# Kernel optimization log

Hardware: AMD Instinct MI355X
Metric: run time of the kernel (lower is better)

The kernel has to match this reference:

```python
import jax, jax.numpy as jnp
import numpy as np

B, NR, NA, NF = 2, 768, 768, 16
RIN, AIN = 1024, 1024
DIM, HEADS, DHEAD, DEPTH = 512, 8, 64, 4
INNER = HEADS * DHEAD
IFF = int(DIM * 4 * 2 / 3)  # 1365, GEGLU inner dim


def _ln(x, g, b=None):
    mu = jnp.mean(x, axis=-1, keepdims=True)
    var = jnp.mean((x - mu) ** 2, axis=-1, keepdims=True)
    y = (x - mu) * jax.lax.rsqrt(var + 1e-5) * g
    return y if b is None else y + b


def _heads(t):
    b, n, _ = t.shape
    return t.reshape(b, n, HEADS, DHEAD).transpose(0, 2, 1, 3)  # b h n d


def _attend(qx, kvx, wq, wkv, wo, mask):
    q = _heads(qx @ wq) * (DHEAD ** -0.5)
    k, v = map(_heads, jnp.split(kvx @ wkv, 2, axis=-1))
    sim = jnp.einsum('bhid,bhjd->bhij', q, k)
    sim = jnp.where(mask, sim, -jnp.finfo(sim.dtype).max)
    attn = jax.nn.softmax(sim, axis=-1)
    out = jnp.einsum('bhij,bhjd->bhid', attn, v)
    out = out.transpose(0, 2, 1, 3).reshape(qx.shape[0], -1, INNER)
    return out @ wo


def _masks():
    # token types: RNA=0, FUSION=2, ATAC=1, laid out [rna | fusion | atac]
    types = jnp.concatenate([jnp.zeros(NR, jnp.int32), jnp.full((NF,), 2, jnp.int32), jnp.ones(NA, jnp.int32)])
    same = (types[:, None] == types[None, :]).astype(jnp.int32)
    # replicates torch source precedence: (zorro_mask | types_from) == FUSION
    zorro = (same | types[:, None]) == 2
    rt = jnp.arange(3, dtype=jnp.int32)  # return token types (RNA, ATAC, FUSION)
    pm = (rt[:, None] == types[None, :]).astype(jnp.int32)
    # replicates source precedence: (pool_mask | return_types) == GLOBAL(3)
    pool = (pm | rt[:, None]) == 3
    return zorro[None, None], pool[None, None]


def setup_inputs() -> dict:
    key = jax.random.key(0)
    ks = jax.random.split(key, 16)
    w = lambda k, s: jax.random.normal(k, s, jnp.float32) * 0.02
    return {
        'rna': jax.random.normal(ks[0], (B, NR, RIN), jnp.float32),
        'atac': jax.random.normal(ks[1], (B, NA, AIN), jnp.float32),
        'rna_ln1_g': jnp.ones((RIN,)), 'rna_ln1_b': jnp.zeros((RIN,)),
        'rna_w': w(ks[2], (RIN, DIM)), 'rna_b': jnp.zeros((DIM,)),
        'rna_ln2_g': jnp.ones((DIM,)), 'rna_ln2_b': jnp.zeros((DIM,)),
        'atac_ln1_g': jnp.ones((AIN,)), 'atac_ln1_b': jnp.zeros((AIN,)),
        'atac_w': w(ks[3], (AIN, DIM)), 'atac_b': jnp.zeros((DIM,)),
        'atac_ln2_g': jnp.ones((DIM,)), 'atac_ln2_b': jnp.zeros((DIM,)),
        'fusion_tokens': jax.random.normal(ks[4], (NF, DIM), jnp.float32),
        'layers_attn_g': jnp.ones((DEPTH, DIM)),
        'layers_wq': w(ks[5], (DEPTH, DIM, INNER)),
        'layers_wkv': w(ks[6], (DEPTH, DIM, 2 * INNER)),
        'layers_wo': w(ks[7], (DEPTH, INNER, DIM)),
        'layers_ff_g': jnp.ones((DEPTH, DIM)),
        'layers_ff_w1': w(ks[8], (DEPTH, DIM, 2 * IFF)),
        'layers_ff_w2': w(ks[9], (DEPTH, IFF, DIM)),
        'final_g': jnp.ones((DIM,)),
        'return_tokens': jax.random.normal(ks[10], (3, DIM), jnp.float32),
        'pool_g': jnp.ones((DIM,)),
        'pool_wq': w(ks[11], (DIM, INNER)),
        'pool_wkv': w(ks[12], (DIM, 2 * INNER)),
        'pool_wo': w(ks[13], (INNER, DIM)),
    }


def reference(rna, atac, rna_ln1_g, rna_ln1_b, rna_w, rna_b, rna_ln2_g, rna_ln2_b,
              atac_ln1_g, atac_ln1_b, atac_w, atac_b, atac_ln2_g, atac_ln2_b,
              fusion_tokens, layers_attn_g, layers_wq, layers_wkv, layers_wo,
              layers_ff_g, layers_ff_w1, layers_ff_w2, final_g, return_tokens,
              pool_g, pool_wq, pool_wkv, pool_wo):
    zorro_mask, pool_mask = _masks()
    rna_tok = _ln(_ln(rna, rna_ln1_g, rna_ln1_b) @ rna_w + rna_b, rna_ln2_g, rna_ln2_b)
    atac_tok = _ln(_ln(atac, atac_ln1_g, atac_ln1_b) @ atac_w + atac_b, atac_ln2_g, atac_ln2_b)
    fus = jnp.broadcast_to(fusion_tokens, (B, NF, DIM))
    tokens = jnp.concatenate([rna_tok, fus, atac_tok], axis=1)  # [B, N, DIM]

    def layer(tok, p):
        ag, wq, wkv, wo, fg, w1, w2 = p
        xn = _ln(tok, ag)
        tok = tok + _attend(xn, xn, wq, wkv, wo, zorro_mask)
        h = _ln(tok, fg) @ w1
        x1, gate = jnp.split(h, 2, axis=-1)
        tok = tok + (jax.nn.gelu(gate, approximate=False) * x1) @ w2
        return tok, None

    tokens, _ = jax.lax.scan(layer, tokens,
                             (layers_attn_g, layers_wq, layers_wkv, layers_wo,
                              layers_ff_g, layers_ff_w1, layers_ff_w2))
    tokens = _ln(tokens, final_g)
    ret = jnp.broadcast_to(return_tokens, (B, 3, DIM))
    pooled = _attend(_ln(ret, pool_g), tokens, pool_wq, pool_wkv, pool_wo, pool_mask) + ret
    return pooled
```

## Files before the change

### kernel.cpp

```cpp
#include <hip/hip_runtime.h>
#include <stdint.h>
#include <stddef.h>

#define NTOK 1552
#define DIMM 512
#define IFFC 1365
#define IFF2 2730
#define NW1 2816
#define GSTRIDE 1408
#define BATCH 2
#define MALL (BATCH*NTOK)
#define AZ 6

typedef unsigned short u16;
typedef __attribute__((ext_vector_type(8))) short bf16x8;
typedef __attribute__((ext_vector_type(4))) float f32x4;

__device__ __forceinline__ u16 f2bf(float f){
  union { float f; uint32_t u; } v; v.f = f;
  uint32_t u = v.u;
  uint32_t r = (u + 0x7FFFu + ((u >> 16) & 1u)) >> 16;
  return (u16)r;
}
__device__ __forceinline__ float bf2f(u16 x){
  union { uint32_t u; float f; } v; v.u = ((uint32_t)x) << 16; return v.f;
}

__device__ __forceinline__ void gload_lds16(const u16* g, u16* l){
  __builtin_amdgcn_global_load_lds((const __attribute__((address_space(1))) void*)g,
                                   (__attribute__((address_space(3))) void*)l, 16, 0, 0);
}

__global__ void convall(const float* s0,const float* s1,const float* s2,const float* s3,
                        const float* s4,const float* s5,const float* s6,const float* s7,
                        u16* d0,u16* d1,u16* d2,u16* d3,u16* d4,u16* d5,u16* d6,u16* d7)
{
  const float* srcs[8] = {s0,s1,s2,s3,s4,s5,s6,s7};
  u16* dsts[8] = {d0,d1,d2,d3,d4,d5,d6,d7};
  const int KT[8]   = {32,32,16,16,16,16,44,16};
  const int NT[8]   = {16,16,32,16,16,88,16,32};
  const int TC[8]   = {512,512,2048,1024,1024,5632,2816,512};
  const int K_[8]   = {1024,1024,512,512,512,512,1365,512};
  const int NSRC[8] = {512,512,1024,512,512,2730,512,1024};
  const int LDK[8]  = {1024,1024,512,512,512,512,1408,512};
  const int NOUT[8] = {512,512,1024,512,512,2816,512,1024};
  const int WS_[8]  = {0,0,512*1024,512*512,512*512,512*2730,1365*512,0};
  const int WT_[8]  = {0,0,1024*512,512*512,512*512,2816*512,512*1408,0};

  int bid = blockIdx.x;
  int seg = 0, base = 0;
  while (seg < 7 && bid >= base + TC[seg]) { base += TC[seg]; ++seg; }
  int loc = bid - base;
  int kt = KT[seg];
  int z = loc / (kt*NT[seg]); loc -= z*(kt*NT[seg]);
  int kb = (loc % kt) * 32, nb = (loc / kt) * 32;
  const float* w = srcs[seg] + (size_t)z * WS_[seg];
  u16* wt = dsts[seg] + (size_t)z * WT_[seg];
  int K = K_[seg], NS = NSRC[seg], ldk = LDK[seg], NO = NOUT[seg];

  __shared__ float tile[32][33];
  int t = threadIdx.x;
  {
    int k = t >> 3, n4 = (t & 7) * 4;
    int gk = kb + k;
    float4 v = make_float4(0.f,0.f,0.f,0.f);
    if (gk < K){
      if (seg != 5){
        int gn = nb + n4;
        if (gn + 4 <= NS){
          v = *(const float4*)(w + (size_t)gk*NS + gn);
        } else {
          float* pv = (float*)&v;
          #pragma unroll
          for (int i = 0; i < 4; ++i){ int n = gn + i; if (n < NS) pv[i] = w[(size_t)gk*NS + n]; }
        }
      } else {
        float* pv = (float*)&v;
        #pragma unroll
        for (int i = 0; i < 4; ++i){
          int n = nb + n4 + i;
          if (n < NO){
            int bb = n >> 7, rr = n & 127, g = rr >> 5, hh = rr & 31;
            int j = bb*64 + g*16 + (hh & 15);
            if (j < 1365) pv[i] = w[(size_t)gk*NS + ((hh < 16) ? j : 1365 + j)];
          }
        }
      }
    }
    tile[k][n4] = v.x; tile[k][n4+1] = v.y; tile[k][n4+2] = v.z; tile[k][n4+3] = v.w;
  }
  __syncthreads();
  if (t < 128){
    int n = t >> 2, k8 = (t & 3) * 8;
    int gn = nb + n, gk = kb + k8;
    if (gn < NO && gk < ldk){
      u16 sh[8];
      #pragma unroll
      for (int i = 0; i < 8; ++i) sh[i] = f2bf(tile[k8+i][n]);
      *(bf16x8*)(wt + (size_t)gn*ldk + gk) = *(bf16x8*)sh;
    }
  }
}

__global__ void embed_ln1(const float* __restrict__ rna, const float* __restrict__ atac,
                          const float* __restrict__ g0, const float* __restrict__ b0,
                          const float* __restrict__ g1, const float* __restrict__ b1,
                          u16* __restrict__ out)
{
  int r = blockIdx.x;
  const float* x; const float* g; const float* bb;
  if (r < 1536){ x = rna + (size_t)r*1024; g = g0; bb = b0; }
  else { x = atac + (size_t)(r-1536)*1024; g = g1; bb = b1; }
  float s = 0.f, ss = 0.f;
  int t = threadIdx.x;
  float v0 = x[t], v1 = x[t+256], v2 = x[t+512], v3 = x[t+768];
  s = v0+v1+v2+v3; ss = v0*v0+v1*v1+v2*v2+v3*v3;
  #pragma unroll
  for (int off = 32; off >= 1; off >>= 1){ s += __shfl_xor(s, off); ss += __shfl_xor(ss, off); }
  __shared__ float rs_[4], rss_[4];
  int w = t >> 6;
  if ((t & 63) == 0){ rs_[w] = s; rss_[w] = ss; }
  __syncthreads();
  s = rs_[0]+rs_[1]+rs_[2]+rs_[3];
  ss = rss_[0]+rss_[1]+rss_[2]+rss_[3];
  float mu = s / 1024.f;
  float rstd = rsqrtf(ss / 1024.f - mu*mu + 1e-5f);
  u16* o = out + (size_t)r*1024;
  o[t]     = f2bf((v0-mu)*rstd*g[t]     + bb[t]);
  o[t+256] = f2bf((v1-mu)*rstd*g[t+256] + bb[t+256]);
  o[t+512] = f2bf((v2-mu)*rstd*g[t+512] + bb[t+512]);
  o[t+768] = f2bf((v3-mu)*rstd*g[t+768] + bb[t+768]);
}

__global__ void embed_addln2(const float* __restrict__ part,
                             const float* __restrict__ rb, const float* __restrict__ ab,
                             const float* __restrict__ g0, const float* __restrict__ bt0,
                             const float* __restrict__ g1, const float* __restrict__ bt1,
                             const float* __restrict__ ag0,
                             float* __restrict__ tok, u16* __restrict__ xn)
{
  int r = blockIdx.x;
  int mod = (r >= 1536);
  int rl = mod ? r - 1536 : r;
  int b = rl / 768, rr = rl % 768;
  const float* bias = mod ? ab : rb;
  const float* g = mod ? g1 : g0;
  const float* bt = mod ? bt1 : bt0;
  const float* p0 = part + (size_t)r*DIMM;
  const float* p1 = p0 + (size_t)3072*DIMM;
  int t = threadIdx.x;
  float v0 = p0[t] + p1[t] + bias[t];
  float v1 = p0[t+256] + p1[t+256] + bias[t+256];
  float s = v0 + v1, ss = v0*v0 + v1*v1;
  #pragma unroll
  for (int off = 32; off >= 1; off >>= 1){ s += __shfl_xor(s, off); ss += __shfl_xor(ss, off); }
  __shared__ float rs_[4], rss_[4];
  int w = t >> 6;
  if ((t & 63) == 0){ rs_[w] = s; rss_[w] = ss; }
  __syncthreads();
  s = rs_[0]+rs_[1]+rs_[2]+rs_[3];
  ss = rss_[0]+rss_[1]+rss_[2]+rss_[3];
  float mu = s / DIMM;
  float rstd = rsqrtf(ss / DIMM - mu*mu + 1e-5f);
  size_t row = (size_t)(b*NTOK + (mod ? 784 : 0) + rr)*DIMM;
  float t0 = (v0 - mu)*rstd*g[t]     + bt[t];
  float t1 = (v1 - mu)*rstd*g[t+256] + bt[t+256];
  tok[row + t] = t0; tok[row + t+256] = t1;
  float s2 = t0 + t1, ss2 = t0*t0 + t1*t1;
  #pragma unroll
  for (int off = 32; off >= 1; off >>= 1){ s2 += __shfl_xor(s2, off); ss2 += __shfl_xor(ss2, off); }
  __syncthreads();
  if ((t & 63) == 0){ rs_[w] = s2; rss_[w] = ss2; }
  __syncthreads();
  s2 = rs_[0]+rs_[1]+rs_[2]+rs_[3];
  ss2 = rss_[0]+rss_[1]+rss_[2]+rss_[3];
  float mu2 = s2 / DIMM;
  float rstd2 = rsqrtf(ss2 / DIMM - mu2*mu2 + 1e-5f);
  xn[row + t]     = f2bf((t0 - mu2)*rstd2*ag0[t]);
  xn[row + t+256] = f2bf((t1 - mu2)*rstd2*ag0[t+256]);
}

__global__ void fuscopy_ln(const float* __restrict__ ft, const float* __restrict__ ag0,
                           float* __restrict__ tok, u16* __restrict__ xn)
{
  int bid = blockIdx.x;
  int b = bid >> 4, rr = bid & 15;
  int t = threadIdx.x;
  const float* x = ft + (size_t)rr*DIMM;
  float v0 = x[t], v1 = x[t+256];
  size_t row = (size_t)(b*NTOK + 768 + rr)*DIMM;
  tok[row + t] = v0; tok[row + t+256] = v1;
  float s = v0 + v1, ss = v0*v0 + v1*v1;
  #pragma unroll
  for (int off = 32; off >= 1; off >>= 1){ s += __shfl_xor(s, off); ss += __shfl_xor(ss, off); }
  __shared__ float rs_[4], rss_[4];
  int w = t >> 6;
  if ((t & 63) == 0){ rs_[w] = s; rss_[w] = ss; }
  __syncthreads();
  s = rs_[0]+rs_[1]+rs_[2]+rs_[3];
  ss = rss_[0]+rss_[1]+rss_[2]+rss_[3];
  float mu = s / DIMM;
  float rstd = rsqrtf(ss / DIMM - mu*mu + 1e-5f);
  xn[row + t]     = f2bf((v0 - mu)*rstd*ag0[t]);
  xn[row + t+256] = f2bf((v1 - mu)*rstd*ag0[t+256]);
}

__global__ void resadd_ffnln(float* __restrict__ tok, const float* __restrict__ proj,
                             const float* __restrict__ g, u16* __restrict__ xn)
{
  int n = blockIdx.x, b = blockIdx.y;
  int pr = (n >= 768 && n < 784) ? (1 + n - 768) : 0;
  const float* p = proj + ((size_t)b*17 + pr)*DIMM;
  size_t row = (size_t)(b*NTOK + n)*DIMM;
  int t = threadIdx.x;
  float v0 = tok[row + t]     + p[t];
  float v1 = tok[row + t+256] + p[t+256];
  tok[row + t] = v0; tok[row + t+256] = v1;
  float s = v0 + v1, ss = v0*v0 + v1*v1;
  #pragma unroll
  for (int off = 32; off >= 1; off >>= 1){ s += __shfl_xor(s, off); ss += __shfl_xor(ss, off); }
  __shared__ float rs_[4], rss_[4];
  int w = t >> 6;
  if ((t & 63) == 0){ rs_[w] = s; rss_[w] = ss; }
  __syncthreads();
  s = rs_[0]+rs_[1]+rs_[2]+rs_[3];
  ss = rss_[0]+rss_[1]+rss_[2]+rss_[3];
  float mu = s / DIMM;
  float rstd = rsqrtf(ss / DIMM - mu*mu + 1e-5f);
  xn[row + t]     = f2bf((v0 - mu)*rstd*g[t]);
  xn[row + t+256] = f2bf((v1 - mu)*rstd*g[t+256]);
}

__global__ void skadd_ln(float* __restrict__ tok, const float* __restrict__ part,
                         const float* __restrict__ g, u16* __restrict__ xn)
{
  int r = blockIdx.x;
  size_t row = (size_t)r*DIMM;
  const float* p0 = part + row;
  const float* p1 = p0 + (size_t)MALL*DIMM;
  int t = threadIdx.x;
  float v0 = tok[row + t]     + p0[t]     + p1[t];
  float v1 = tok[row + t+256] + p0[t+256] + p1[t+256];
  tok[row + t] = v0; tok[row + t+256] = v1;
  float s = v0 + v1, ss = v0*v0 + v1*v1;
  #pragma unroll
  for (int off = 32; off >= 1; off >>= 1){ s += __shfl_xor(s, off); ss += __shfl_xor(ss, off); }
  __shared__ float rs_[4], rss_[4];
  int w = t >> 6;
  if ((t & 63) == 0){ rs_[w] = s; rss_[w] = ss; }
  __syncthreads();
  s = rs_[0]+rs_[1]+rs_[2]+rs_[3];
  ss = rss_[0]+rss_[1]+rss_[2]+rss_[3];
  float mu = s / DIMM;
  float rstd = rsqrtf(ss / DIMM - mu*mu + 1e-5f);
  xn[row + t]     = f2bf((v0 - mu)*rstd*g[t]);
  xn[row + t+256] = f2bf((v1 - mu)*rstd*g[t+256]);
}

__global__ __launch_bounds__(512) void gemm512(
    const u16* __restrict__ A, int lda,
    const u16* __restrict__ Bt, const u16* __restrict__ BtB, int mswitch, int ldk,
    float* __restrict__ C, int ldc, size_t Cz,
    u16* __restrict__ gout, float* __restrict__ csum,
    int M, int Nn, int K, int kchunk)
{
  __shared__ __align__(16) u16 As_lin[2][128*32];
  __shared__ __align__(16) u16 Bs_lin[2][128*32];
  __shared__ float colsum[2][128];
  const int t = threadIdx.x;
  const int lane = t & 63;
  const int w = t >> 6;
  const int wr = (w >> 2) * 64;
  const int wc = (w & 3) * 32;
  const int row0 = blockIdx.x * 128, col0 = blockIdx.y * 128;
  if (BtB && row0 >= mswitch) Bt = BtB;
  const int z = blockIdx.z;
  const int kbeg = z * kchunk;
  const int kend = (kbeg + kchunk < K) ? (kbeg + kchunk) : K;
  C += (size_t)z * Cz;
  const int l15 = lane & 15;
  const int l4 = (lane >> 4) * 8;
  const int sr = t >> 2, sc8 = (t & 3) * 8;
  int gr_s = row0 + sr; if (gr_s >= M) gr_s = M - 1;
  int gc_s = col0 + sr; if (gc_s >= Nn) gc_s = Nn - 1;
  const u16* Ag = A + (size_t)gr_s*lda + sc8;
  const u16* Bg = Bt + (size_t)gc_s*ldk + sc8;
  const int wb = w * 512;

  f32x4 acc[4][2];
  #pragma unroll
  for (int m = 0; m < 4; ++m)
    #pragma unroll
    for (int n = 0; n < 2; ++n)
      #pragma unroll
      for (int j = 0; j < 4; ++j) acc[m][n][j] = 0.f;

  gload_lds16(Ag + kbeg, &As_lin[0][wb]);
  gload_lds16(Bg + kbeg, &Bs_lin[0][wb]);
  __syncthreads();

  int cur = 0;
  for (int k0 = kbeg; k0 < kend; k0 += 32) {
    int k1 = k0 + 32;
    if (k1 < kend){
      gload_lds16(Ag + k1, &As_lin[cur^1][wb]);
      gload_lds16(Bg + k1, &Bs_lin[cur^1][wb]);
    }
    const u16* Ar = &As_lin[cur][0];
    const u16* Br = &Bs_lin[cur][0];
    bf16x8 af[4], bfr[2];
    #pragma unroll
    for (int m = 0; m < 4; ++m) af[m]  = *(const bf16x8*)(&Ar[(wr + m*16 + l15)*32 + l4]);
    #pragma unroll
    for (int n = 0; n < 2; ++n) bfr[n] = *(const bf16x8*)(&Br[(wc + n*16 + l15)*32 + l4]);
    #pragma unroll
    for (int m = 0; m < 4; ++m)
      #pragma unroll
      for (int n = 0; n < 2; ++n)
        acc[m][n] = __builtin_amdgcn_mfma_f32_16x16x32_bf16(af[m], bfr[n], acc[m][n], 0, 0, 0);
    __syncthreads();
    cur ^= 1;
  }
  const int rb = (lane >> 4) * 4;
  if (gout){
    int jcol = (col0 >> 1) + (w & 3)*16 + l15;
    #pragma unroll
    for (int m = 0; m < 4; ++m){
      int gr0 = row0 + wr + m*16 + rb;
      #pragma unroll
      for (int j = 0; j < 4; ++j){
        int gr = gr0 + j;
        if (gr < M){
          float gt = acc[m][1][j];
          float ge = 0.5f * gt * (1.0f + erff(gt * 0.70710678118654752f));
          gout[(size_t)gr*GSTRIDE + jcol] = f2bf(ge * acc[m][0][j]);
        }
      }
    }
  } else {
    #pragma unroll
    for (int m = 0; m < 4; ++m){
      int gr0 = row0 + wr + m*16 + rb;
      #pragma unroll
      for (int n = 0; n < 2; ++n){
        int gc = col0 + wc + n*16 + l15;
        if (gc >= Nn) continue;
        #pragma unroll
        for (int j = 0; j < 4; ++j){
          int gr = gr0 + j;
          if (gr < M) C[(size_t)gr*ldc + gc] = acc[m][n][j];
        }
      }
    }
  }
  if (csum && col0 >= 512){
    if (t < 256) colsum[t>>7][t&127] = 0.f;
    __syncthreads();
    #pragma unroll
    for (int n = 0; n < 2; ++n){
      float lv0 = 0.f, lv1 = 0.f;
      #pragma unroll
      for (int m = 0; m < 4; ++m){
        int gr0 = row0 + wr + m*16 + rb;
        #pragma unroll
        for (int j = 0; j < 4; ++j){
          float v = acc[m][n][j];
          if (gr0 + j < NTOK) lv0 += v; else lv1 += v;
        }
      }
      int lc = wc + n*16 + l15;
      atomicAdd(&colsum[0][lc], lv0);
      atomicAdd(&colsum[1][lc], lv1);
    }
    __syncthreads();
    if (t < 256){
      int bb = t>>7, c = t&127;
      csum[((size_t)(bb*25) + blockIdx.x)*512 + (col0 - 512) + c] = colsum[bb][c];
    }
  }
}

__global__ __launch_bounds__(256) void fused_attn(
    const u16* __restrict__ xn, const u16* __restrict__ wqt,
    const float* __restrict__ kv, float* __restrict__ apart)
{
  int h = blockIdx.x, b = blockIdx.y;
  int qi = blockIdx.z / AZ, jz = blockIdx.z % AZ;
  int t = threadIdx.x;
  int lane = t & 63, wid = t >> 6;
  __shared__ float xs[512];
  __shared__ float qs[64];
  __shared__ float pl[256];
  __shared__ float red[4][64];
  __shared__ float redm[4];

  {
    int row = b*NTOK + 768 + qi;
    const u16* xr = xn + (size_t)row*DIMM;
    xs[t] = bf2f(xr[t]);
    xs[t+256] = bf2f(xr[t+256]);
  }
  __syncthreads();

  {
    const u16* wrr = wqt + (size_t)(h*64 + lane)*DIMM + wid*128;
    float a = 0.f;
    #pragma unroll
    for (int k = 0; k < 128; k += 8){
      bf16x8 wv = *(const bf16x8*)(wrr + k);
      int kb = wid*128 + k;
      #pragma unroll
      for (int i = 0; i < 8; ++i) a += xs[kb+i] * bf2f((u16)wv[i]);
    }
    red[wid][lane] = a;
  }
  __syncthreads();
  if (t < 64) qs[t] = (red[0][t] + red[1][t] + red[2][t] + red[3][t]) * 0.125f;
  __syncthreads();

  int jj = jz*256 + t;
  int j = (jj < 768) ? jj : jj + 16;
  float a = 0.f;
  {
    const float* kr = kv + ((size_t)(b*NTOK + j))*1024 + h*64;
    #pragma unroll
    for (int d = 0; d < 64; d += 4){
      float4 kd = *(const float4*)(kr + d);
      a += qs[d]*kd.x + qs[d+1]*kd.y + qs[d+2]*kd.z + qs[d+3]*kd.w;
    }
  }

  float m = a;
  #pragma unroll
  for (int off = 32; off >= 1; off >>= 1) m = fmaxf(m, __shfl_xor(m, off));
  if (lane == 0) redm[wid] = m;
  __syncthreads();
  m = fmaxf(fmaxf(redm[0], redm[1]), fmaxf(redm[2], redm[3]));
  float p = __expf(a - m);
  pl[t] = p;
  float sq = p;
  #pragma unroll
  for (int off = 32; off >= 1; off >>= 1) sq += __shfl_xor(sq, off);
  if (lane == 0) redm[wid] = sq;
  __syncthreads();

  {
    int j0 = wid * 64;
    const float* vb = kv + ((size_t)(b*NTOK + jz*256 + j0 + ((jz*256 + j0 >= 768) ? 16 : 0)))*1024
                      + 512 + h*64 + lane;
    float a0=0.f, a1=0.f, a2=0.f, a3=0.f;
    #pragma unroll 4
    for (int i = 0; i < 64; i += 4){
      const float* vp = vb + (size_t)i*1024;
      a0 += pl[j0+i]   * vp[0];
      a1 += pl[j0+i+1] * vp[1024];
      a2 += pl[j0+i+2] * vp[2048];
      a3 += pl[j0+i+3] * vp[3072];
    }
    red[wid][lane] = a0+a1+a2+a3;
  }
  __syncthreads();
  float* po = apart + ((((size_t)jz*BATCH + b)*8 + h)*16 + qi) * 68;
  if (t < 64) po[t] = red[0][t] + red[1][t] + red[2][t] + red[3][t];
  else if (t == 64) po[64] = m;
  else if (t == 65) po[65] = redm[0] + redm[1] + redm[2] + redm[3];
}

__global__ __launch_bounds__(256) void attn_out(
    const float* __restrict__ apart, const float* __restrict__ csum,
    const u16* __restrict__ wot, float* __restrict__ proj)
{
  int colchunk = blockIdx.x;
  int b = blockIdx.y;
  int rg = blockIdx.z;
  int r0 = (rg == 0) ? 0 : (1 + 4*rg);
  int nr = (rg == 0) ? 5 : 4;
  __shared__ float zbl[5][512];
  __shared__ float red[4][64];
  int t = threadIdx.x;

  for (int rr = 0; rr < nr; ++rr){
    int r = r0 + rr;
    if (r == 0){
      for (int c = t; c < 512; c += 256){
        float s = 0.f;
        #pragma unroll
        for (int bx = 0; bx < 25; ++bx) s += csum[((size_t)(b*25)+bx)*512 + c];
        zbl[rr][c] = s * (1.0f/1552.0f);
      }
    } else {
      int qi = r - 1;
      for (int c = t; c < 512; c += 256){
        int h = c >> 6, d = c & 63;
        size_t base = ((size_t)b*8 + h)*16 + qi;
        float mz[AZ], sz[AZ];
        float M = -3.4e38f;
        #pragma unroll
        for (int z = 0; z < AZ; ++z){
          const float* po = apart + ((size_t)z*BATCH*8*16 + base)*68;
          mz[z] = po[64]; sz[z] = po[65];
          M = fmaxf(M, mz[z]);
        }
        float S = 0.f, O = 0.f;
        #pragma unroll
        for (int z = 0; z < AZ; ++z){
          const float* po = apart + ((size_t)z*BATCH*8*16 + base)*68;
          float wz = __expf(mz[z] - M);
          S += sz[z]*wz; O += po[d]*wz;
        }
        zbl[rr][c] = O / S;
      }
    }
  }
  __syncthreads();

  int col = colchunk*64 + (t & 63);
  int kq = t >> 6;
  const u16* wrow = wot + (size_t)col*512 + kq*128;
  for (int rr = 0; rr < nr; ++rr){
    float a = 0.f;
    #pragma unroll
    for (int k = 0; k < 128; k += 8){
      bf16x8 wv = *(const bf16x8*)(wrow + k);
      #pragma unroll
      for (int i = 0; i < 8; ++i) a += zbl[rr][kq*128 + k + i] * bf2f((u16)wv[i]);
    }
    red[kq][t & 63] = a;
    __syncthreads();
    if (t < 64)
      proj[((size_t)(b*17) + r0 + rr)*DIMM + colchunk*64 + t] =
        red[0][t] + red[1][t] + red[2][t] + red[3][t];
    __syncthreads();
  }
}

__global__ __launch_bounds__(256) void pool_final(
    const float* __restrict__ csum, const float* __restrict__ rt,
    const float* __restrict__ pg, const float* __restrict__ wq,
    const float* __restrict__ kv, const float* __restrict__ wo,
    float* __restrict__ out)
{
  int colchunk = blockIdx.x;
  int br = blockIdx.y; int b = br/3, r = br%3;
  __shared__ float ys[512];
  __shared__ float q2l[512];
  __shared__ float qred[2][512];
  __shared__ float fred[16][64];
  __shared__ float sm[8][16];
  __shared__ float pn[8][16];
  __shared__ float rs_[4], rss_[4];
  int t = threadIdx.x;

  if (r < 2){
    float a0 = 0.f, a1 = 0.f;
    #pragma unroll
    for (int bx = 0; bx < 25; ++bx){
      a0 += csum[((size_t)(b*25)+bx)*512 + t];
      a1 += csum[((size_t)(b*25)+bx)*512 + t + 256];
    }
    ys[t] = a0 * (1.0f/1552.0f);
    ys[t+256] = a1 * (1.0f/1552.0f);
    __syncthreads();
  } else {
    const float* x = rt + 2*DIMM;
    float v0 = x[t], v1 = x[t+256];
    float s = v0 + v1, ss = v0*v0 + v1*v1;
    #pragma unroll
    for (int off = 32; off >= 1; off >>= 1){ s += __shfl_xor(s, off); ss += __shfl_xor(ss, off); }
    int w = t >> 6;
    if ((t & 63) == 0){ rs_[w] = s; rss_[w] = ss; }
    __syncthreads();
    s = rs_[0]+rs_[1]+rs_[2]+rs_[3];
    ss = rss_[0]+rss_[1]+rss_[2]+rss_[3];
    float mu = s / DIMM;
    float rstd = rsqrtf(ss / DIMM - mu*mu + 1e-5f);
    ys[t]     = (v0 - mu)*rstd*pg[t];
    ys[t+256] = (v1 - mu)*rstd*pg[t+256];
    __syncthreads();
    {
      int c4 = (t & 127) * 4;
      int kq = t >> 7;
      float ax=0.f, ay=0.f, az=0.f, aw=0.f;
      #pragma unroll 8
      for (int k = kq*256; k < kq*256 + 256; ++k){
        float yv = ys[k];
        float4 w4 = *(const float4*)(wq + (size_t)k*512 + c4);
        ax += yv*w4.x; ay += yv*w4.y; az += yv*w4.z; aw += yv*w4.w;
      }
      qred[kq][c4] = ax; qred[kq][c4+1] = ay; qred[kq][c4+2] = az; qred[kq][c4+3] = aw;
    }
    __syncthreads();
    q2l[t]     = (qred[0][t]     + qred[1][t])     * 0.125f;
    q2l[t+256] = (qred[0][t+256] + qred[1][t+256]) * 0.125f;
    __syncthreads();
    if (t < 128){
      int h = t >> 4, j = t & 15;
      const float* kr = kv + ((size_t)(b*NTOK + 768 + j))*1024 + h*64;
      float a = 0.f;
      #pragma unroll
      for (int d = 0; d < 64; ++d) a += q2l[h*64 + d] * kr[d];
      sm[h][j] = a;
    }
    __syncthreads();
    if (t < 8){
      float m = -3.4e38f;
      #pragma unroll
      for (int j = 0; j < 16; ++j) m = fmaxf(m, sm[t][j]);
      float e[16]; float s2 = 0.f;
      #pragma unroll
      for (int j = 0; j < 16; ++j){ e[j] = __expf(sm[t][j] - m); s2 += e[j]; }
      float inv = 1.0f / s2;
      #pragma unroll
      for (int j = 0; j < 16; ++j) pn[t][j] = e[j] * inv;
    }
    __syncthreads();
    {
      int c0 = t, c1 = t + 256;
      int h0 = c0 >> 6, h1 = c1 >> 6;
      float a0 = 0.f, a1 = 0.f;
      #pragma unroll
      for (int j = 0; j < 16; ++j){
        const float* vr = kv + ((size_t)(b*NTOK + 768 + j))*1024 + 512;
        a0 += pn[h0][j] * vr[c0];
        a1 += pn[h1][j] * vr[c1];
      }
      ys[c0] = a0; ys[c1] = a1;
    }
    __syncthreads();
  }

  {
    int c4l = (t & 15) * 4;
    int c4 = colchunk*64 + c4l;
    int kq = t >> 4;
    float ax=0.f, ay=0.f, az=0.f, aw=0.f;
    #pragma unroll 8
    for (int k = kq*32; k < kq*32 + 32; ++k){
      float yv = ys[k];
      float4 w4 = *(const float4*)(wo + (size_t)k*512 + c4);
      ax += yv*w4.x; ay += yv*w4.y; az += yv*w4.z; aw += yv*w4.w;
    }
    fred[kq][c4l] = ax; fred[kq][c4l+1] = ay; fred[kq][c4l+2] = az; fred[kq][c4l+3] = aw;
  }
  __syncthreads();
  if (t < 64){
    float a = 0.f;
    #pragma unroll
    for (int kq = 0; kq < 16; ++kq) a += fred[kq][t];
    int c = colchunk*64 + t;
    out[(size_t)br*DIMM + c] = a + rt[(size_t)r*DIMM + c];
  }
}

extern "C" void kernel_launch(void* const* d_in, const int* in_sizes, int n_in,
                              void* d_out, int out_size, void* d_ws, size_t ws_size,
                              hipStream_t stream)
{
  const float* rna        = (const float*)d_in[0];
  const float* atac       = (const float*)d_in[1];
  const float* rna_ln1_g  = (const float*)d_in[2];
  const float* rna_ln1_b  = (const float*)d_in[3];
  const float* rna_w      = (const float*)d_in[4];
  const float* rna_b      = (const float*)d_in[5];
  const float* rna_ln2_g  = (const float*)d_in[6];
  const float* rna_ln2_b  = (const float*)d_in[7];
  const float* atac_ln1_g = (const float*)d_in[8];
  const float* atac_ln1_b = (const float*)d_in[9];
  const float* atac_w     = (const float*)d_in[10];
  const float* atac_b     = (const float*)d_in[11];
  const float* atac_ln2_g = (const float*)d_in[12];
  const float* atac_ln2_b = (const float*)d_in[13];
  const float* fusion_tok = (const float*)d_in[14];
  const float* lay_ag     = (const float*)d_in[15];
  const float* lay_wq     = (const float*)d_in[16];
  const float* lay_wkv    = (const float*)d_in[17];
  const float* lay_wo     = (const float*)d_in[18];
  const float* lay_fg     = (const float*)d_in[19];
  const float* lay_w1     = (const float*)d_in[20];
  const float* lay_w2     = (const float*)d_in[21];
  const float* final_g    = (const float*)d_in[22];
  const float* ret_tok    = (const float*)d_in[23];
  const float* pool_g     = (const float*)d_in[24];
  const float* pool_wq    = (const float*)d_in[25];
  const float* pool_wkv   = (const float*)d_in[26];
  const float* pool_wo    = (const float*)d_in[27];

  uint8_t* ws = (uint8_t*)d_ws;
  size_t off = 0;
  auto carve = [&](size_t bytes) -> uint8_t* {
    uint8_t* p = ws + off;
    off += (bytes + 255) & ~(size_t)255;
    return p;
  };
  u16* rna_wt   = (u16*)carve((size_t)512*1024*2);
  u16* atac_wt  = (u16*)carve((size_t)512*1024*2);
  u16* wkvt     = (u16*)carve((size_t)4*1024*512*2);
  u16* wqt      = (u16*)carve((size_t)4*512*512*2);
  u16* wot      = (u16*)carve((size_t)4*512*512*2);
  u16* w1t      = (u16*)carve((size_t)4*NW1*512*2);
  u16* w2t      = (u16*)carve((size_t)4*512*GSTRIDE*2);
  u16* pool_wkvt= (u16*)carve((size_t)1024*512*2);
  float* tok   = (float*)carve((size_t)MALL * DIMM * 4);
  u16*   xn    = (u16*)  carve((size_t)MALL * DIMM * 2);
  float* kv    = (float*)carve((size_t)MALL * 1024 * 4);
  u16*   lnbuf = (u16*)  carve((size_t)3072 * 1024 * 2);
  float* proj  = (float*)carve((size_t)BATCH*17*DIMM * 4);
  float* csum  = (float*)carve((size_t)BATCH*25*512 * 4);
  float* apart = (float*)carve((size_t)AZ*BATCH*8*16*68 * 4);
  u16*   gbuf  = (u16*)  carve((size_t)MALL * GSTRIDE * 2);
  float* skpart= (float*)carve((size_t)2 * MALL * 512 * 4);
  (void)ws_size;

  convall<<<14080, 256, 0, stream>>>(rna_w, atac_w, lay_wkv, lay_wq, lay_wo, lay_w1, lay_w2, pool_wkv,
                                     rna_wt, atac_wt, wkvt, wqt, wot, w1t, w2t, pool_wkvt);

  embed_ln1<<<3072, 256, 0, stream>>>(rna, atac, rna_ln1_g, rna_ln1_b, atac_ln1_g, atac_ln1_b, lnbuf);
  gemm512<<<dim3(24, 4, 2), 512, 0, stream>>>(lnbuf, 1024, rna_wt, atac_wt, 1536, 1024,
                                              skpart, 512, (size_t)3072*512, nullptr, nullptr,
                                              3072, 512, 1024, 512);
  embed_addln2<<<3072, 256, 0, stream>>>(skpart, rna_b, atac_b, rna_ln2_g, rna_ln2_b,
                                         atac_ln2_g, atac_ln2_b, lay_ag, tok, xn);
  fuscopy_ln<<<32, 256, 0, stream>>>(fusion_tok, lay_ag, tok, xn);

  for (int l = 0; l < 4; ++l){
    const float* fg  = lay_fg + (size_t)l*DIMM;
    const float* gnext = (l < 3) ? (lay_ag + (size_t)(l+1)*DIMM) : final_g;
    const u16* wkvt_l = wkvt + (size_t)l*1024*512;
    const u16* wqt_l  = wqt  + (size_t)l*512*512;
    const u16* wot_l  = wot  + (size_t)l*512*512;
    const u16* w1t_l  = w1t  + (size_t)l*NW1*512;
    const u16* w2t_l  = w2t  + (size_t)l*512*GSTRIDE;

    gemm512<<<dim3(25, 8, 1), 512, 0, stream>>>(xn, 512, wkvt_l, nullptr, 0, 512,
                                                kv, 1024, 0, nullptr, csum, MALL, 1024, 512, 512);
    fused_attn<<<dim3(8, BATCH, 16*AZ), 256, 0, stream>>>(xn, wqt_l, kv, apart);
    attn_out<<<dim3(8, BATCH, 4), 256, 0, stream>>>(apart, csum, wot_l, proj);
    resadd_ffnln<<<dim3(NTOK, BATCH), 256, 0, stream>>>(tok, proj, fg, xn);
    gemm512<<<dim3(25, 22, 1), 512, 0, stream>>>(xn, 512, w1t_l, nullptr, 0, 512,
                                                 nullptr, 0, 0, gbuf, nullptr, MALL, NW1, 512, 512);
    gemm512<<<dim3(25, 4, 2), 512, 0, stream>>>(gbuf, GSTRIDE, w2t_l, nullptr, 0, GSTRIDE,
                                                skpart, 512, (size_t)MALL*512, nullptr, nullptr,
                                                MALL, 512, GSTRIDE, 704);
    skadd_ln<<<MALL, 256, 0, stream>>>(tok, skpart, gnext, xn);
  }

  gemm512<<<dim3(25, 8, 1), 512, 0, stream>>>(xn, 512, pool_wkvt, nullptr, 0, 512,
                                              kv, 1024, 0, nullptr, csum, MALL, 1024, 512, 512);
  pool_final<<<dim3(8, 6), 256, 0, stream>>>(csum, ret_tok, pool_g, pool_wq, kv, pool_wo,
                                             (float*)d_out);
}
```

Measured before the change: 540.6 us.

## Merge prep kernels and raise split-K for embed and FFN-down GEMMs

Folds the embedding LayerNorm into the weight-conversion launch and the fusion-token copy into embed_addln2, cutting two kernel launches. It also raises split-K for the embedding GEMM from 2 to 4 and for the W2 GEMM from 2 to 3 (K chunk 480), so these small grids fill more compute units. The reduction kernels now sum more partial buffers, which adds memory traffic. The W2 split of 3×480 covers K=1408 only if the GEMM clamps the last chunk.

Result: faster. 525.5 us (-2.8%).

```diff
diff --git a/kernel.cpp b/kernel.cpp
--- a/kernel.cpp
+++ b/kernel.cpp
@@ -11,6 +11,8 @@
 #define BATCH 2
 #define MALL (BATCH*NTOK)
 #define AZ 6
+#define W2SK 3
+#define EMSK 4
 
 typedef unsigned short u16;
 typedef __attribute__((ext_vector_type(8))) short bf16x8;
@@ -31,10 +33,39 @@
                                    (__attribute__((address_space(3))) void*)l, 16, 0, 0);
 }
 
-__global__ void convall(const float* s0,const float* s1,const float* s2,const float* s3,
-                        const float* s4,const float* s5,const float* s6,const float* s7,
-                        u16* d0,u16* d1,u16* d2,u16* d3,u16* d4,u16* d5,u16* d6,u16* d7)
-{
+__global__ void prep_kernel(const float* s0,const float* s1,const float* s2,const float* s3,
+                            const float* s4,const float* s5,const float* s6,const float* s7,
+                            u16* d0,u16* d1,u16* d2,u16* d3,u16* d4,u16* d5,u16* d6,u16* d7,
+                            const float* rna, const float* atac,
+                            const float* g0e, const float* b0e,
+                            const float* g1e, const float* b1e, u16* lnout)
+{
+  __shared__ float tile[32][33];
+  __shared__ float rs_[4], rss_[4];
+  int t = threadIdx.x;
+  if (blockIdx.x >= 14080){
+    int r = blockIdx.x - 14080;
+    const float* x; const float* g; const float* bb;
+    if (r < 1536){ x = rna + (size_t)r*1024; g = g0e; bb = b0e; }
+    else { x = atac + (size_t)(r-1536)*1024; g = g1e; bb = b1e; }
+    float v0 = x[t], v1 = x[t+256], v2 = x[t+512], v3 = x[t+768];
+    float s = v0+v1+v2+v3, ss = v0*v0+v1*v1+v2*v2+v3*v3;
+    #pragma unroll
+    for (int off = 32; off >= 1; off >>= 1){ s += __shfl_xor(s, off); ss += __shfl_xor(ss, off); }
+    int w = t >> 6;
+    if ((t & 63) == 0){ rs_[w] = s; rss_[w] = ss; }
+    __syncthreads();
+    s = rs_[0]+rs_[1]+rs_[2]+rs_[3];
+    ss = rss_[0]+rss_[1]+rss_[2]+rss_[3];
+    float mu = s / 1024.f;
+    float rstd = rsqrtf(ss / 1024.f - mu*mu + 1e-5f);
+    u16* o = lnout + (size_t)r*1024;
+    o[t]     = f2bf((v0-mu)*rstd*g[t]     + bb[t]);
+    o[t+256] = f2bf((v1-mu)*rstd*g[t+256] + bb[t+256]);
+    o[t+512] = f2bf((v2-mu)*rstd*g[t+512] + bb[t+512]);
+    o[t+768] = f2bf((v3-mu)*rstd*g[t+768] + bb[t+768]);
+    return;
+  }
   const float* srcs[8] = {s0,s1,s2,s3,s4,s5,s6,s7};
   u16* dsts[8] = {d0,d1,d2,d3,d4,d5,d6,d7};
   const int KT[8]   = {32,32,16,16,16,16,44,16};
@@ -58,8 +89,6 @@
   u16* wt = dsts[seg] + (size_t)z * WT_[seg];
   int K = K_[seg], NS = NSRC[seg], ldk = LDK[seg], NO = NOUT[seg];
 
-  __shared__ float tile[32][33];
-  int t = threadIdx.x;
   {
     int k = t >> 3, n4 = (t & 7) * 4;
     int gk = kb + k;
@@ -102,44 +131,38 @@
   }
 }
 
-__global__ void embed_ln1(const float* __restrict__ rna, const float* __restrict__ atac,
-                          const float* __restrict__ g0, const float* __restrict__ b0,
-                          const float* __restrict__ g1, const float* __restrict__ b1,
-                          u16* __restrict__ out)
-{
-  int r = blockIdx.x;
-  const float* x; const float* g; const float* bb;
-  if (r < 1536){ x = rna + (size_t)r*1024; g = g0; bb = b0; }
-  else { x = atac + (size_t)(r-1536)*1024; g = g1; bb = b1; }
-  float s = 0.f, ss = 0.f;
-  int t = threadIdx.x;
-  float v0 = x[t], v1 = x[t+256], v2 = x[t+512], v3 = x[t+768];
-  s = v0+v1+v2+v3; ss = v0*v0+v1*v1+v2*v2+v3*v3;
-  #pragma unroll
-  for (int off = 32; off >= 1; off >>= 1){ s += __shfl_xor(s, off); ss += __shfl_xor(ss, off); }
-  __shared__ float rs_[4], rss_[4];
-  int w = t >> 6;
-  if ((t & 63) == 0){ rs_[w] = s; rss_[w] = ss; }
-  __syncthreads();
-  s = rs_[0]+rs_[1]+rs_[2]+rs_[3];
-  ss = rss_[0]+rss_[1]+rss_[2]+rss_[3];
-  float mu = s / 1024.f;
-  float rstd = rsqrtf(ss / 1024.f - mu*mu + 1e-5f);
-  u16* o = out + (size_t)r*1024;
-  o[t]     = f2bf((v0-mu)*rstd*g[t]     + bb[t]);
-  o[t+256] = f2bf((v1-mu)*rstd*g[t+256] + bb[t+256]);
-  o[t+512] = f2bf((v2-mu)*rstd*g[t+512] + bb[t+512]);
-  o[t+768] = f2bf((v3-mu)*rstd*g[t+768] + bb[t+768]);
-}
-
 __global__ void embed_addln2(const float* __restrict__ part,
                              const float* __restrict__ rb, const float* __restrict__ ab,
                              const float* __restrict__ g0, const float* __restrict__ bt0,
                              const float* __restrict__ g1, const float* __restrict__ bt1,
-                             const float* __restrict__ ag0,
+                             const float* __restrict__ ag0, const float* __restrict__ ft,
                              float* __restrict__ tok, u16* __restrict__ xn)
 {
-  int r = blockIdx.x;
+  __shared__ float rs_[4], rss_[4];
+  int t = threadIdx.x;
+  int bid = blockIdx.x;
+  if (bid >= 3072){
+    int idx = bid - 3072;
+    int b = idx >> 4, rr = idx & 15;
+    const float* x = ft + (size_t)rr*DIMM;
+    float v0 = x[t], v1 = x[t+256];
+    size_t row = (size_t)(b*NTOK + 768 + rr)*DIMM;
+    tok[row + t] = v0; tok[row + t+256] = v1;
+    float s = v0 + v1, ss = v0*v0 + v1*v1;
+    #pragma unroll
+    for (int off = 32; off >= 1; off >>= 1){ s += __shfl_xor(s, off); ss += __shfl_xor(ss, off); }
+    int w = t >> 6;
+    if ((t & 63) == 0){ rs_[w] = s; rss_[w] = ss; }
+    __syncthreads();
+    s = rs_[0]+rs_[1]+rs_[2]+rs_[3];
+    ss = rss_[0]+rss_[1]+rss_[2]+rss_[3];
+    float mu = s / DIMM;
+    float rstd = rsqrtf(ss / DIMM - mu*mu + 1e-5f);
+    xn[row + t]     = f2bf((v0 - mu)*rstd*ag0[t]);
+    xn[row + t+256] = f2bf((v1 - mu)*rstd*ag0[t+256]);
+    return;
+  }
+  int r = bid;
   int mod = (r >= 1536);
   int rl = mod ? r - 1536 : r;
   int b = rl / 768, rr = rl % 768;
@@ -147,14 +170,15 @@
   const float* g = mod ? g1 : g0;
   const float* bt = mod ? bt1 : bt0;
   const float* p0 = part + (size_t)r*DIMM;
-  const float* p1 = p0 + (size_t)3072*DIMM;
-  int t = threadIdx.x;
-  float v0 = p0[t] + p1[t] + bias[t];
-  float v1 = p0[t+256] + p1[t+256] + bias[t+256];
+  float v0 = bias[t], v1 = bias[t+256];
+  #pragma unroll
+  for (int z = 0; z < EMSK; ++z){
+    const float* pz = p0 + (size_t)z*3072*DIMM;
+    v0 += pz[t]; v1 += pz[t+256];
+  }
   float s = v0 + v1, ss = v0*v0 + v1*v1;
   #pragma unroll
   for (int off = 32; off >= 1; off >>= 1){ s += __shfl_xor(s, off); ss += __shfl_xor(ss, off); }
-  __shared__ float rs_[4], rss_[4];
   int w = t >> 6;
   if ((t & 63) == 0){ rs_[w] = s; rss_[w] = ss; }
   __syncthreads();
@@ -180,31 +204,6 @@
   xn[row + t+256] = f2bf((t1 - mu2)*rstd2*ag0[t+256]);
 }
 
-__global__ void fuscopy_ln(const float* __restrict__ ft, const float* __restrict__ ag0,
-                           float* __restrict__ tok, u16* __restrict__ xn)
-{
-  int bid = blockIdx.x;
-  int b = bid >> 4, rr = bid & 15;
-  int t = threadIdx.x;
-  const float* x = ft + (size_t)rr*DIMM;
-  float v0 = x[t], v1 = x[t+256];
-  size_t row = (size_t)(b*NTOK + 768 + rr)*DIMM;
-  tok[row + t] = v0; tok[row + t+256] = v1;
-  float s = v0 + v1, ss = v0*v0 + v1*v1;
-  #pragma unroll
-  for (int off = 32; off >= 1; off >>= 1){ s += __shfl_xor(s, off); ss += __shfl_xor(ss, off); }
-  __shared__ float rs_[4], rss_[4];
-  int w = t >> 6;
-  if ((t & 63) == 0){ rs_[w] = s; rss_[w] = ss; }
-  __syncthreads();
-  s = rs_[0]+rs_[1]+rs_[2]+rs_[3];
-  ss = rss_[0]+rss_[1]+rss_[2]+rss_[3];
-  float mu = s / DIMM;
-  float rstd = rsqrtf(ss / DIMM - mu*mu + 1e-5f);
-  xn[row + t]     = f2bf((v0 - mu)*rstd*ag0[t]);
-  xn[row + t+256] = f2bf((v1 - mu)*rstd*ag0[t+256]);
-}
-
 __global__ void resadd_ffnln(float* __restrict__ tok, const float* __restrict__ proj,
                              const float* __restrict__ g, u16* __restrict__ xn)
 {
@@ -236,11 +235,13 @@
 {
   int r = blockIdx.x;
   size_t row = (size_t)r*DIMM;
-  const float* p0 = part + row;
-  const float* p1 = p0 + (size_t)MALL*DIMM;
   int t = threadIdx.x;
-  float v0 = tok[row + t]     + p0[t]     + p1[t];
-  float v1 = tok[row + t+256] + p0[t+256] + p1[t+256];
+  float v0 = tok[row + t], v1 = tok[row + t+256];
+  #pragma unroll
+  for (int z = 0; z < W2SK; ++z){
+    const float* pz = part + (size_t)z*MALL*DIMM + row;
+    v0 += pz[t]; v1 += pz[t+256];
+  }
   tok[row + t] = v0; tok[row + t+256] = v1;
   float s = v0 + v1, ss = v0*v0 + v1*v1;
   #pragma unroll
@@ -708,19 +709,20 @@
   float* csum  = (float*)carve((size_t)BATCH*25*512 * 4);
   float* apart = (float*)carve((size_t)AZ*BATCH*8*16*68 * 4);
   u16*   gbuf  = (u16*)  carve((size_t)MALL * GSTRIDE * 2);
-  float* skpart= (float*)carve((size_t)2 * MALL * 512 * 4);
+  size_t skelems = (size_t)EMSK*3072*512;
+  float* skpart= (float*)carve(skelems * 4);
   (void)ws_size;
 
-  convall<<<14080, 256, 0, stream>>>(rna_w, atac_w, lay_wkv, lay_wq, lay_wo, lay_w1, lay_w2, pool_wkv,
-                                     rna_wt, atac_wt, wkvt, wqt, wot, w1t, w2t, pool_wkvt);
-
-  embed_ln1<<<3072, 256, 0, stream>>>(rna, atac, rna_ln1_g, rna_ln1_b, atac_ln1_g, atac_ln1_b, lnbuf);
-  gemm512<<<dim3(24, 4, 2), 512, 0, stream>>>(lnbuf, 1024, rna_wt, atac_wt, 1536, 1024,
-                                              skpart, 512, (size_t)3072*512, nullptr, nullptr,
-                                              3072, 512, 1024, 512);
-  embed_addln2<<<3072, 256, 0, stream>>>(skpart, rna_b, atac_b, rna_ln2_g, rna_ln2_b,
-                                         atac_ln2_g, atac_ln2_b, lay_ag, tok, xn);
-  fuscopy_ln<<<32, 256, 0, stream>>>(fusion_tok, lay_ag, tok, xn);
+  prep_kernel<<<14080 + 3072, 256, 0, stream>>>(
+      rna_w, atac_w, lay_wkv, lay_wq, lay_wo, lay_w1, lay_w2, pool_wkv,
+      rna_wt, atac_wt, wkvt, wqt, wot, w1t, w2t, pool_wkvt,
+      rna, atac, rna_ln1_g, rna_ln1_b, atac_ln1_g, atac_ln1_b, lnbuf);
+
+  gemm512<<<dim3(24, 4, EMSK), 512, 0, stream>>>(lnbuf, 1024, rna_wt, atac_wt, 1536, 1024,
+                                                 skpart, 512, (size_t)3072*512, nullptr, nullptr,
+                                                 3072, 512, 1024, 1024/EMSK);
+  embed_addln2<<<3104, 256, 0, stream>>>(skpart, rna_b, atac_b, rna_ln2_g, rna_ln2_b,
+                                         atac_ln2_g, atac_ln2_b, lay_ag, fusion_tok, tok, xn);
 
   for (int l = 0; l < 4; ++l){
     const float* fg  = lay_fg + (size_t)l*DIMM;
@@ -738,9 +740,9 @@
     resadd_ffnln<<<dim3(NTOK, BATCH), 256, 0, stream>>>(tok, proj, fg, xn);
     gemm512<<<dim3(25, 22, 1), 512, 0, stream>>>(xn, 512, w1t_l, nullptr, 0, 512,
                                                  nullptr, 0, 0, gbuf, nullptr, MALL, NW1, 512, 512);
-    gemm512<<<dim3(25, 4, 2), 512, 0, stream>>>(gbuf, GSTRIDE, w2t_l, nullptr, 0, GSTRIDE,
-                                                skpart, 512, (size_t)MALL*512, nullptr, nullptr,
-                                                MALL, 512, GSTRIDE, 704);
+    gemm512<<<dim3(25, 4, W2SK), 512, 0, stream>>>(gbuf, GSTRIDE, w2t_l, nullptr, 0, GSTRIDE,
+                                                   skpart, 512, (size_t)MALL*512, nullptr, nullptr,
+                                                   MALL, 512, GSTRIDE, 480);
     skadd_ln<<<MALL, 256, 0, stream>>>(tok, skpart, gnext, xn);
   }
 
```
